# Kernel optimization log

Measured on AMD Instinct MI355X. Metric: run time of the kernel, lower is better.

## Reference

```python
import jax, jax.numpy as jnp
import numpy as np

# Ragged layout: 8 sequences packed into total_tokens=6144 tokens.
_SEQLENS = [1024, 512, 1024, 256, 768, 1024, 512, 1024]
_TOTAL = sum(_SEQLENS)  # 6144
_H, _D = 16, 128
_MAXLEN = 1024


def setup_inputs() -> dict:
    key = jax.random.key(0)
    kq, kk, kv = jax.random.split(key, 3)
    cu = jnp.asarray(np.concatenate([[0], np.cumsum(_SEQLENS)]), dtype=jnp.int32)
    return {
        "q": jax.random.normal(kq, (_TOTAL, _H, _D), dtype=jnp.float32),
        "k": jax.random.normal(kk, (_TOTAL, _H, _D), dtype=jnp.float32),
        "v": jax.random.normal(kv, (_TOTAL, _H, _D), dtype=jnp.float32),
        "cu_seqlens_q": cu,
        "cu_seqlens_k": cu,
        "max_seqlen_q": _MAXLEN,
        "max_seqlen_k": _MAXLEN,
    }


def _pad_gather(x, cu, L):
    """Gather packed [T,h,d] into padded [B,L,h,d] plus validity mask [B,L]."""
    starts = cu[:-1]                                   # [B]
    lens = cu[1:] - cu[:-1]                            # [B]
    pos = jnp.arange(L, dtype=cu.dtype)                # [L]
    idx = starts[:, None] + pos[None, :]               # [B,L]
    mask = pos[None, :] < lens[:, None]                # [B,L]
    idx = jnp.clip(idx, 0, x.shape[0] - 1)
    return x[idx], mask, jnp.where(mask, idx, x.shape[0])


def reference(q, k, v, cu_seqlens_q, cu_seqlens_k, max_seqlen_q, max_seqlen_k):
    # Equivalent to pytorch_varlen_attention: per-sequence SDPA (non-causal,
    # no dropout), vectorized via pad-to-max + key masking.
    T, h, d = q.shape
    qp, mq, idx_q = _pad_gather(q, cu_seqlens_q, max_seqlen_q)  # [B,Lq,h,d]
    kp, mk, _ = _pad_gather(k, cu_seqlens_k, max_seqlen_k)      # [B,Lk,h,d]
    vp, _, _ = _pad_gather(v, cu_seqlens_k, max_seqlen_k)

    scale = 1.0 / jnp.sqrt(jnp.asarray(d, dtype=q.dtype))
    scores = jnp.einsum("bqhd,bkhd->bhqk", qp, kp) * scale      # [B,h,Lq,Lk]
    neg = jnp.asarray(jnp.finfo(scores.dtype).min, scores.dtype)
    scores = jnp.where(mk[:, None, None, :], scores, neg)
    attn = jax.nn.softmax(scores, axis=-1)
    out_pad = jnp.einsum("bhqk,bkhd->bqhd", attn, vp)           # [B,Lq,h,d]

    # Scatter valid rows back to packed layout; invalid rows dropped (idx==T).
    out = jnp.zeros((T, h, d), dtype=q.dtype)
    out = out.at[idx_q.reshape(-1)].set(
        out_pad.reshape(-1, h, d), mode="drop")
    return out
```

## Files before the change

kernel.cpp:

```cpp
#include <hip/hip_runtime.h>
#include <hip/hip_bf16.h>
#include <stdint.h>

#define H 16
#define D 128
#define BM 256
#define BN 64
#define NW 8
#define NT 512

typedef __bf16 bf16_t;
typedef bf16_t bf16x8 __attribute__((ext_vector_type(8)));
typedef bf16_t bf16x2 __attribute__((ext_vector_type(2)));
typedef float f32x16 __attribute__((ext_vector_type(16)));

#define MFMA32(a, b, c) __builtin_amdgcn_mfma_f32_32x32x16_bf16(a, b, c, 0, 0, 0)

union FragU { uint32_t w[4]; bf16x8 v; };

static __device__ __forceinline__ uint32_t cvtpk_bf16(float lo, float hi) {
  uint32_t r;
  asm("v_cvt_pk_bf16_f32 %0, %1, %2" : "=v"(r) : "v"(lo), "v"(hi));
  return r;
}

static __device__ __forceinline__ void gld_lds16(const bf16_t* g, bf16_t* l) {
  __builtin_amdgcn_global_load_lds(
      (const __attribute__((address_space(1))) void*)g,
      (__attribute__((address_space(3))) void*)l, 16, 0, 0);
}


__global__ void conv_k(const float* __restrict__ kin, bf16_t* __restrict__ kb, int n8) {
  int i = blockIdx.x * blockDim.x + threadIdx.x;
  int stride = gridDim.x * blockDim.x;
  for (; i < n8; i += stride) {
    const float* p = kin + (size_t)i * 8;
    float4 a = *(const float4*)p, b = *(const float4*)(p + 4);
    bf16x8 w;
    w[0] = (bf16_t)a.x; w[1] = (bf16_t)a.y; w[2] = (bf16_t)a.z; w[3] = (bf16_t)a.w;
    w[4] = (bf16_t)b.x; w[5] = (bf16_t)b.y; w[6] = (bf16_t)b.z; w[7] = (bf16_t)b.w;
    *(bf16x8*)(kb + (size_t)i * 8) = w;
  }
}

__global__ void conv_vt(const float* __restrict__ v, bf16_t* __restrict__ vt,
                        const int* __restrict__ cuk, int nseq) {
  int tile = blockIdx.x, h = blockIdx.y;
  int acc = 0, seq = -1, lt = 0, s0k = 0, Lk = 0, Lkp = 0;
  size_t vb = 0;
  for (int s = 0; s < nseq; ++s) {
    int Ls = cuk[s + 1] - cuk[s];
    int Lp = (Ls + 63) & ~63;
    int nt = Lp / 64;
    if (tile < acc + nt) { seq = s; lt = tile - acc; s0k = cuk[s]; Lk = Ls; Lkp = Lp; break; }
    acc += nt; vb += (size_t)H * D * Lp;
  }
  if (seq < 0) return;
  int kv0 = lt * 64;
  int d = threadIdx.x;
  bf16x8 w[8];
  #pragma unroll
  for (int j = 0; j < 64; ++j) {
    int kv = kv0 + j;
    int kvc = kv < Lk ? kv : Lk - 1;
    float val = v[((size_t)(s0k + kvc) * H + h) * D + d];
    w[j >> 3][j & 7] = (bf16_t)val;
  }
  bf16_t* dstT = vt + vb + (size_t)h * D * Lkp + (size_t)lt * 8192;
  #pragma unroll
  for (int c = 0; c < 8; ++c)
    *(bf16x8*)(dstT + ((size_t)c * 128 + d) * 8) = w[c];
}


__global__ __launch_bounds__(NT, 2)
void fa_varlen8(const float* __restrict__ q,
                const bf16_t* __restrict__ kb,
                const bf16_t* __restrict__ vt,
                const int* __restrict__ cuq,
                const int* __restrict__ cuk,
                float* __restrict__ out,
                int nseq, int maxtiles)
{
  __shared__ alignas(16) bf16_t sK[2][BN * D];
  __shared__ alignas(16) bf16_t sVt[2][8 * 128 * 8];
  __shared__ float sRed[NW * 32];

  const int nwg = gridDim.x;
  const int orig = blockIdx.x;
  const int qq = nwg >> 3, rr = nwg & 7;
  const int xcd = orig & 7;
  const int wgid = (xcd < rr ? xcd * (qq + 1) : rr * (qq + 1) + (xcd - rr) * qq) + (orig >> 3);
  const int tile = wgid % maxtiles;
  const int h = wgid / maxtiles;

  int acc = 0, seq = -1, lt = 0, s0q = 0, s0k = 0, Lq = 0, Lk = 0, Lkp = 0;
  size_t vb = 0;
  for (int s = 0; s < nseq; ++s) {
    int a = cuq[s], b = cuq[s + 1];
    int Ls = b - a;
    int nt = (Ls + BM - 1) / BM;
    int Lks = cuk[s + 1] - cuk[s];
    int Lp = (Lks + 63) & ~63;
    if (tile < acc + nt) {
      seq = s; lt = tile - acc; s0q = a; Lq = Ls;
      s0k = cuk[s]; Lk = Lks; Lkp = Lp;
      break;
    }
    acc += nt; vb += (size_t)H * D * Lp;
  }
  if (seq < 0) return;

  const int q0 = lt * BM;
  const int tid = threadIdx.x;
  const int warp = tid >> 6;
  const int lane = tid & 63;
  const int lq = lane & 31;
  const int hi = lane >> 5;

  const float SC = 0.08838834764831845f * 1.44269504088896340f;

  bf16x8 qf[8];
  {
    int qrow = q0 + warp * 32 + lq; if (qrow >= Lq) qrow = Lq - 1;
    const float* qp = q + ((size_t)(s0q + qrow) * H + h) * D;
    #pragma unroll
    for (int ks = 0; ks < 8; ++ks) {
      const float* p = qp + ks * 16 + hi * 8;
      float4 a = *(const float4*)p, b = *(const float4*)(p + 4);
      bf16x8 r;
      r[0] = (bf16_t)(a.x * SC); r[1] = (bf16_t)(a.y * SC);
      r[2] = (bf16_t)(a.z * SC); r[3] = (bf16_t)(a.w * SC);
      r[4] = (bf16_t)(b.x * SC); r[5] = (bf16_t)(b.y * SC);
      r[6] = (bf16_t)(b.z * SC); r[7] = (bf16_t)(b.w * SC);
      qf[ks] = r;
    }
  }

  const bf16_t* vsrcH = vt + vb + (size_t)h * D * Lkp;

  auto STAGE = [&](int tt, int buf) {
    const int kvb = tt * BN;
    #pragma unroll
    for (int i = 0; i < 2; ++i) {
      int g = tid + i * NT;
      int row = g >> 4, cc = g & 15;
      int kvr = kvb + row; if (kvr >= Lk) kvr = Lk - 1;
      const bf16_t* src = kb + ((size_t)(s0k + kvr) * H + h) * D + ((cc ^ (row & 7)) << 3);
      gld_lds16(src, &sK[buf][g * 8]);
    }
    const bf16_t* vsrc = vsrcH + (size_t)tt * 8192;
    #pragma unroll
    for (int i = 0; i < 2; ++i) {
      int g = tid + i * NT;
      gld_lds16(vsrc + (size_t)g * 8, &sVt[buf][g * 8]);
    }
  };

  f32x16 oacc[4];
  #pragma unroll
  for (int dt = 0; dt < 4; ++dt)
    #pragma unroll
    for (int r = 0; r < 16; ++r) oacc[dt][r] = 0.f;
  float m = -1e30f, l = 0.f;

  const int nkv = (Lk + BN - 1) / BN;

  STAGE(0, 0);
  asm volatile("s_waitcnt vmcnt(0)" ::: "memory");
  __syncthreads();

  for (int t = 0; t < nkv; ++t) {
    const int cur = t & 1;
    const int kvb = t * BN;
    if (t + 1 < nkv) STAGE(t + 1, cur ^ 1);

    const bf16_t* sKc = sK[cur];
    const bf16_t* sVc = sVt[cur];
    const bool tail = (kvb + BN > Lk);

    #pragma unroll
    for (int ct = 0; ct < 2; ++ct) {
      f32x16 sa, sb;
      #pragma unroll
      for (int r = 0; r < 16; ++r) { sa[r] = 0.f; sb[r] = 0.f; }
      int krow = ct * 32 + lq;
      __builtin_amdgcn_s_setprio(1);
      #pragma unroll
      for (int ks = 0; ks < 4; ++ks) {
        int posa = (ks * 2 + hi) ^ (krow & 7);
        bf16x8 kfa = *(const bf16x8*)&sKc[krow * 128 + (posa << 3)];
        sa = MFMA32(kfa, qf[ks], sa);
        int posb = ((ks + 4) * 2 + hi) ^ (krow & 7);
        bf16x8 kfb = *(const bf16x8*)&sKc[krow * 128 + (posb << 3)];
        sb = MFMA32(kfb, qf[ks + 4], sb);
      }
      __builtin_amdgcn_s_setprio(0);

      f32x16 st;
      #pragma unroll
      for (int r = 0; r < 16; ++r) {
        float x = sa[r] + sb[r];
        if (tail) {
          int kvi = kvb + ct * 32 + (r & 3) + 8 * (r >> 2) + 4 * hi;
          if (kvi >= Lk) x = -1e30f;
        }
        st[r] = x;
      }
      float m0, m1;
      {
        float a0 = fmaxf(st[0], st[1]),  a1 = fmaxf(st[2], st[3]);
        float a2 = fmaxf(st[4], st[5]),  a3 = fmaxf(st[6], st[7]);
        float a4 = fmaxf(st[8], st[9]),  a5 = fmaxf(st[10], st[11]);
        float a6 = fmaxf(st[12], st[13]), a7 = fmaxf(st[14], st[15]);
        float b0 = fmaxf(a0, a1), b1 = fmaxf(a2, a3);
        float b2 = fmaxf(a4, a5), b3 = fmaxf(a6, a7);
        m0 = fmaxf(fmaxf(b0, b1), fmaxf(b2, b3));
      }
      m1 = fmaxf(m0, __shfl_xor(m0, 32));
      bool trig = m1 > m + 8.0f;
      float mnew = trig ? m1 : m;
      float alpha = __builtin_amdgcn_exp2f(m - mnew);
      m = mnew;

      #pragma unroll
      for (int r = 0; r < 16; ++r)
        st[r] = __builtin_amdgcn_exp2f(st[r] - m);
      float psum;
      {
        float a0 = st[0] + st[1],  a1 = st[2] + st[3];
        float a2 = st[4] + st[5],  a3 = st[6] + st[7];
        float a4 = st[8] + st[9],  a5 = st[10] + st[11];
        float a6 = st[12] + st[13], a7 = st[14] + st[15];
        float b0 = a0 + a1, b1 = a2 + a3, b2 = a4 + a5, b3 = a6 + a7;
        psum = (b0 + b1) + (b2 + b3);
      }
      psum += __shfl_xor(psum, 32);
      l = l * alpha + psum;

      if (__any(alpha != 1.0f)) {
        if (hi == 0) sRed[warp * 32 + lq] = alpha;
        asm volatile("s_waitcnt lgkmcnt(0)" ::: "memory");
        #pragma unroll
        for (int r = 0; r < 16; ++r) {
          float a2 = sRed[warp * 32 + (r & 3) + 8 * (r >> 2) + 4 * hi];
          #pragma unroll
          for (int dt = 0; dt < 4; ++dt) oacc[dt][r] *= a2;
        }
      }

      uint32_t c0 = cvtpk_bf16(st[0],  st[1]),  c1 = cvtpk_bf16(st[2],  st[3]);
      uint32_t c2 = cvtpk_bf16(st[4],  st[5]),  c3 = cvtpk_bf16(st[6],  st[7]);
      uint32_t c4 = cvtpk_bf16(st[8],  st[9]),  c5 = cvtpk_bf16(st[10], st[11]);
      uint32_t c6 = cvtpk_bf16(st[12], st[13]), c7 = cvtpk_bf16(st[14], st[15]);
      { auto rr2 = __builtin_amdgcn_permlane32_swap(c0, c2, false, false); c0 = rr2[0]; c2 = rr2[1]; }
      { auto rr2 = __builtin_amdgcn_permlane32_swap(c1, c3, false, false); c1 = rr2[0]; c3 = rr2[1]; }
      { auto rr2 = __builtin_amdgcn_permlane32_swap(c4, c6, false, false); c4 = rr2[0]; c6 = rr2[1]; }
      { auto rr2 = __builtin_amdgcn_permlane32_swap(c5, c7, false, false); c5 = rr2[0]; c7 = rr2[1]; }
      FragU pa, pb;
      pa.w[0] = c0; pa.w[1] = c1; pa.w[2] = c2; pa.w[3] = c3;
      pb.w[0] = c4; pb.w[1] = c5; pb.w[2] = c6; pb.w[3] = c7;

      __builtin_amdgcn_s_setprio(1);
      #pragma unroll
      for (int dt = 0; dt < 4; ++dt) {
        int drow = dt * 32 + lq;
        bf16x8 vf0 = *(const bf16x8*)&sVc[((ct * 4 + hi) * 128 + drow) << 3];
        oacc[dt] = MFMA32(pa.v, vf0, oacc[dt]);
        bf16x8 vf1 = *(const bf16x8*)&sVc[((ct * 4 + 2 + hi) * 128 + drow) << 3];
        oacc[dt] = MFMA32(pb.v, vf1, oacc[dt]);
      }
      __builtin_amdgcn_s_setprio(0);
    }

    asm volatile("s_waitcnt vmcnt(0)" ::: "memory");
    __syncthreads();
  }

  if (hi == 0) sRed[warp * 32 + lq] = l;
  asm volatile("s_waitcnt lgkmcnt(0)" ::: "memory");
  #pragma unroll
  for (int r = 0; r < 16; ++r) {
    int cr = (r & 3) + 8 * (r >> 2) + 4 * hi;
    int qr = q0 + warp * 32 + cr;
    if (qr < Lq) {
      float rn = 1.0f / sRed[warp * 32 + cr];
      float* op = out + ((size_t)(s0q + qr) * H + h) * D + lq;
      #pragma unroll
      for (int dt = 0; dt < 4; ++dt)
        op[dt * 32] = oacc[dt][r] * rn;
    }
  }
}


__global__ __launch_bounds__(256, 3)
void fa_varlen2(const float* __restrict__ q,
                const float* __restrict__ k,
                const float* __restrict__ v,
                const int* __restrict__ cuq,
                const int* __restrict__ cuk,
                float* __restrict__ out,
                int nseq)
{
  __shared__ alignas(16) bf16_t sBuf[128 * 128];
  __shared__ float sRed[4 * 32];
  bf16_t* sK  = sBuf;
  bf16_t* sVt = sBuf + 64 * 128;

  const int tile = blockIdx.x;
  const int h = blockIdx.y;

  int acc = 0, seq = -1, lt = 0, s0q = 0, s0k = 0, Lq = 0, Lk = 0;
  for (int s = 0; s < nseq; ++s) {
    int a = cuq[s], b = cuq[s + 1];
    int Ls = b - a;
    int nt = (Ls + 127) / 128;
    if (tile < acc + nt) {
      seq = s; lt = tile - acc; s0q = a; Lq = Ls;
      s0k = cuk[s]; Lk = cuk[s + 1] - s0k;
      break;
    }
    acc += nt;
  }
  if (seq < 0) return;

  const int q0 = lt * 128;
  const int tid = threadIdx.x;
  const int warp = tid >> 6;
  const int lane = tid & 63;
  const int lq = lane & 31;
  const int hi = lane >> 5;

  const float SC = 0.08838834764831845f * 1.44269504088896340f;

  #pragma unroll
  for (int ii = 0; ii < 8; ++ii) {
    int g = tid + ii * 256;
    int row = g >> 4, cc = g & 15;
    int gr = q0 + row; if (gr >= Lq) gr = Lq - 1;
    const float* p = q + ((size_t)(s0q + gr) * H + h) * D + cc * 8;
    float4 f0 = *(const float4*)p;
    float4 f1 = *(const float4*)(p + 4);
    bf16x8 w;
    w[0] = (bf16_t)f0.x; w[1] = (bf16_t)f0.y; w[2] = (bf16_t)f0.z; w[3] = (bf16_t)f0.w;
    w[4] = (bf16_t)f1.x; w[5] = (bf16_t)f1.y; w[6] = (bf16_t)f1.z; w[7] = (bf16_t)f1.w;
    *(bf16x8*)&sBuf[row * 128 + (((cc ^ (row & 7))) << 3)] = w;
  }
  __syncthreads();

  bf16x8 qf[8];
  {
    int row = warp * 32 + lq;
    #pragma unroll
    for (int ks = 0; ks < 8; ++ks) {
      int pos = (ks * 2 + hi) ^ (row & 7);
      qf[ks] = *(const bf16x8*)&sBuf[row * 128 + (pos << 3)];
    }
  }

  f32x16 oacc[4];
  #pragma unroll
  for (int dt = 0; dt < 4; ++dt)
    #pragma unroll
    for (int r = 0; r < 16; ++r) oacc[dt][r] = 0.f;
  float m = -1e30f, l = 0.f;

  const int nkv = (Lk + 63) / 64;
  for (int it = 0; it < nkv; ++it) {
    const int kv0 = it * 64;
    __syncthreads();

    #pragma unroll
    for (int ii = 0; ii < 4; ++ii) {
      int g = tid + ii * 256;
      int row = g >> 4, cc = g & 15;
      int gr = kv0 + row; if (gr >= Lk) gr = Lk - 1;
      const float* p = k + ((size_t)(s0k + gr) * H + h) * D + cc * 8;
      float4 f0 = *(const float4*)p;
      float4 f1 = *(const float4*)(p + 4);
      bf16x8 w;
      w[0] = (bf16_t)f0.x; w[1] = (bf16_t)f0.y; w[2] = (bf16_t)f0.z; w[3] = (bf16_t)f0.w;
      w[4] = (bf16_t)f1.x; w[5] = (bf16_t)f1.y; w[6] = (bf16_t)f1.z; w[7] = (bf16_t)f1.w;
      *(bf16x8*)&sK[row * 128 + (((cc ^ (row & 7))) << 3)] = w;
    }
    {
      int kp = tid & 31;
      int seg = tid >> 5;
      int r0 = kv0 + 2 * kp, r1 = r0 + 1;
      if (r0 >= Lk) r0 = Lk - 1;
      if (r1 >= Lk) r1 = Lk - 1;
      const float* p0 = v + ((size_t)(s0k + r0) * H + h) * D + seg * 16;
      const float* p1 = v + ((size_t)(s0k + r1) * H + h) * D + seg * 16;
      float va[16], vbf[16];
      *(float4*)&va[0]  = *(const float4*)p0;
      *(float4*)&va[4]  = *(const float4*)(p0 + 4);
      *(float4*)&va[8]  = *(const float4*)(p0 + 8);
      *(float4*)&va[12] = *(const float4*)(p0 + 12);
      *(float4*)&vbf[0]  = *(const float4*)p1;
      *(float4*)&vbf[4]  = *(const float4*)(p1 + 4);
      *(float4*)&vbf[8]  = *(const float4*)(p1 + 8);
      *(float4*)&vbf[12] = *(const float4*)(p1 + 12);
      int kvr = 2 * kp;
      #pragma unroll
      for (int i = 0; i < 16; ++i) {
        int d = seg * 16 + i;
        int pos = (kp >> 2) ^ (d & 7);
        bf16x2 w2; w2[0] = (bf16_t)va[i]; w2[1] = (bf16_t)vbf[i];
        *(bf16x2*)&sVt[d * 64 + (pos << 3) + (kvr & 7)] = w2;
      }
    }
    __syncthreads();

    const bool tail = (kv0 + 64 > Lk);

    #pragma unroll
    for (int ct = 0; ct < 2; ++ct) {
      f32x16 st;
      #pragma unroll
      for (int r = 0; r < 16; ++r) st[r] = 0.f;
      int krow = ct * 32 + lq;
      #pragma unroll
      for (int ks = 0; ks < 8; ++ks) {
        int pos = (ks * 2 + hi) ^ (krow & 7);
        bf16x8 kf = *(const bf16x8*)&sK[krow * 128 + (pos << 3)];
        st = MFMA32(kf, qf[ks], st);
      }

      float tmax = -1e30f;
      #pragma unroll
      for (int r = 0; r < 16; ++r) {
        float x = st[r] * SC;
        if (tail) {
          int kvi = kv0 + ct * 32 + (r & 3) + 8 * (r >> 2) + 4 * hi;
          if (kvi >= Lk) x = -1e30f;
        }
        st[r] = x;
        tmax = fmaxf(tmax, x);
      }
      tmax = fmaxf(tmax, __shfl_xor(tmax, 32));
      bool trig = tmax > m + 8.0f;
      float mnew = trig ? tmax : m;
      float alpha = exp2f(m - mnew);
      m = mnew;

      float psum = 0.f;
      #pragma unroll
      for (int r = 0; r < 16; ++r) {
        float e = exp2f(st[r] - m);
        st[r] = e;
        psum += e;
      }
      psum += __shfl_xor(psum, 32);
      l = l * alpha + psum;

      if (__any(alpha != 1.0f)) {
        if (hi == 0) sRed[warp * 32 + lq] = alpha;
        asm volatile("s_waitcnt lgkmcnt(0)" ::: "memory");
        #pragma unroll
        for (int r = 0; r < 16; ++r) {
          float a2 = sRed[warp * 32 + (r & 3) + 8 * (r >> 2) + 4 * hi];
          #pragma unroll
          for (int dt = 0; dt < 4; ++dt) oacc[dt][r] *= a2;
        }
      }

      uint32_t c0 = cvtpk_bf16(st[0],  st[1]),  c1 = cvtpk_bf16(st[2],  st[3]);
      uint32_t c2 = cvtpk_bf16(st[4],  st[5]),  c3 = cvtpk_bf16(st[6],  st[7]);
      uint32_t c4 = cvtpk_bf16(st[8],  st[9]),  c5 = cvtpk_bf16(st[10], st[11]);
      uint32_t c6 = cvtpk_bf16(st[12], st[13]), c7 = cvtpk_bf16(st[14], st[15]);
      { auto rr2 = __builtin_amdgcn_permlane32_swap(c0, c2, false, false); c0 = rr2[0]; c2 = rr2[1]; }
      { auto rr2 = __builtin_amdgcn_permlane32_swap(c1, c3, false, false); c1 = rr2[0]; c3 = rr2[1]; }
      { auto rr2 = __builtin_amdgcn_permlane32_swap(c4, c6, false, false); c4 = rr2[0]; c6 = rr2[1]; }
      { auto rr2 = __builtin_amdgcn_permlane32_swap(c5, c7, false, false); c5 = rr2[0]; c7 = rr2[1]; }
      FragU pa, pb;
      pa.w[0] = c0; pa.w[1] = c1; pa.w[2] = c2; pa.w[3] = c3;
      pb.w[0] = c4; pb.w[1] = c5; pb.w[2] = c6; pb.w[3] = c7;

      #pragma unroll
      for (int dt = 0; dt < 4; ++dt) {
        int drow = dt * 32 + lq;
        int pos0 = (ct * 4 + hi) ^ (drow & 7);
        bf16x8 vf0 = *(const bf16x8*)&sVt[drow * 64 + (pos0 << 3)];
        oacc[dt] = MFMA32(pa.v, vf0, oacc[dt]);
        int pos1 = (ct * 4 + 2 + hi) ^ (drow & 7);
        bf16x8 vf1 = *(const bf16x8*)&sVt[drow * 64 + (pos1 << 3)];
        oacc[dt] = MFMA32(pb.v, vf1, oacc[dt]);
      }
    }
  }

  if (hi == 0) sRed[warp * 32 + lq] = l;
  asm volatile("s_waitcnt lgkmcnt(0)" ::: "memory");
  #pragma unroll
  for (int r = 0; r < 16; ++r) {
    int cr = (r & 3) + 8 * (r >> 2) + 4 * hi;
    int qr = q0 + warp * 32 + cr;
    if (qr < Lq) {
      float rn = 1.0f / sRed[warp * 32 + cr];
      float* op = out + ((size_t)(s0q + qr) * H + h) * D + lq;
      #pragma unroll
      for (int dt = 0; dt < 4; ++dt)
        op[dt * 32] = oacc[dt][r] * rn;
    }
  }
}

extern "C" void kernel_launch(void* const* d_in, const int* in_sizes, int n_in,
                              void* d_out, int out_size, void* d_ws, size_t ws_size,
                              hipStream_t stream) {
  const float* q = (const float*)d_in[0];
  const float* k = (const float*)d_in[1];
  const float* v = (const float*)d_in[2];
  const int* cuq = (const int*)d_in[3];
  const int* cuk = (const int*)d_in[4];
  float* out = (float*)d_out;

  int total = in_sizes[0] / (H * D);
  int nseq = in_sizes[3] - 1;
  int maxtiles = (total + BM - 1) / BM + nseq;

  size_t needK = (size_t)in_sizes[1] * 2;
  size_t needV = (size_t)in_sizes[2] * 2 + (size_t)nseq * 64 * H * D * 2 + 256;

  if (ws_size >= needK + needV) {
    bf16_t* kb = (bf16_t*)d_ws;
    bf16_t* vtb = (bf16_t*)((char*)d_ws + needK);

    conv_k<<<1024, 256, 0, stream>>>(k, kb, in_sizes[1] / 8);
    int maxvt = (total + 63) / 64 + nseq;
    dim3 gvt(maxvt, H);
    conv_vt<<<gvt, 128, 0, stream>>>(v, vtb, cuk, nseq);
    fa_varlen8<<<dim3(maxtiles * H), NT, 0, stream>>>(q, kb, vtb, cuq, cuk, out, nseq, maxtiles);
  } else {
    int mt2 = (total + 127) / 128 + nseq;
    dim3 grid(mt2, H);
    fa_varlen2<<<grid, 256, 0, stream>>>(q, k, v, cuq, cuk, out, nseq);
  }
}
```

Before: 127.4 us.

## Give each warp two 32-row query tiles to reuse K/V LDS fragments

Halves the warps per workgroup (8 to 4) and has each warp process 64 query rows as two 32-row MFMA tiles. Each K and V fragment read from LDS now feeds two MFMAs, halving LDS read traffic per unit of compute. The cost is doubled accumulator and Q fragment registers, which may lower occupancy or cause spills, and fewer waves are available to hide latency.

```diff
diff --git a/kernel.cpp b/kernel.cpp
--- a/kernel.cpp
+++ b/kernel.cpp
@@ -6,8 +6,8 @@
 #define D 128
 #define BM 256
 #define BN 64
-#define NW 8
-#define NT 512
+#define NW 4
+#define NT 256
 
 typedef __bf16 bf16_t;
 typedef bf16_t bf16x8 __attribute__((ext_vector_type(8)));
@@ -75,7 +75,7 @@
 
 
 __global__ __launch_bounds__(NT, 2)
-void fa_varlen8(const float* __restrict__ q,
+void fa_varlen9(const float* __restrict__ q,
                 const bf16_t* __restrict__ kb,
                 const bf16_t* __restrict__ vt,
                 const int* __restrict__ cuq,
@@ -85,7 +85,7 @@
 {
   __shared__ alignas(16) bf16_t sK[2][BN * D];
   __shared__ alignas(16) bf16_t sVt[2][8 * 128 * 8];
-  __shared__ float sRed[NW * 32];
+  __shared__ float sRed[NW * 64];
 
   const int nwg = gridDim.x;
   const int orig = blockIdx.x;
@@ -121,20 +121,33 @@
 
   const float SC = 0.08838834764831845f * 1.44269504088896340f;
 
-  bf16x8 qf[8];
+  bf16x8 qf0[8], qf1[8];
   {
-    int qrow = q0 + warp * 32 + lq; if (qrow >= Lq) qrow = Lq - 1;
-    const float* qp = q + ((size_t)(s0q + qrow) * H + h) * D;
+    int qr0 = q0 + warp * 64 + lq;      if (qr0 >= Lq) qr0 = Lq - 1;
+    int qr1 = q0 + warp * 64 + 32 + lq; if (qr1 >= Lq) qr1 = Lq - 1;
+    const float* qp0 = q + ((size_t)(s0q + qr0) * H + h) * D;
+    const float* qp1 = q + ((size_t)(s0q + qr1) * H + h) * D;
     #pragma unroll
     for (int ks = 0; ks < 8; ++ks) {
-      const float* p = qp + ks * 16 + hi * 8;
-      float4 a = *(const float4*)p, b = *(const float4*)(p + 4);
+      const float* p0 = qp0 + ks * 16 + hi * 8;
+      float4 a = *(const float4*)p0, b = *(const float4*)(p0 + 4);
       bf16x8 r;
       r[0] = (bf16_t)(a.x * SC); r[1] = (bf16_t)(a.y * SC);
       r[2] = (bf16_t)(a.z * SC); r[3] = (bf16_t)(a.w * SC);
       r[4] = (bf16_t)(b.x * SC); r[5] = (bf16_t)(b.y * SC);
       r[6] = (bf16_t)(b.z * SC); r[7] = (bf16_t)(b.w * SC);
-      qf[ks] = r;
+      qf0[ks] = r;
+    }
+    #pragma unroll
+    for (int ks = 0; ks < 8; ++ks) {
+      const float* p1 = qp1 + ks * 16 + hi * 8;
+      float4 a = *(const float4*)p1, b = *(const float4*)(p1 + 4);
+      bf16x8 r;
+      r[0] = (bf16_t)(a.x * SC); r[1] = (bf16_t)(a.y * SC);
+      r[2] = (bf16_t)(a.z * SC); r[3] = (bf16_t)(a.w * SC);
+      r[4] = (bf16_t)(b.x * SC); r[5] = (bf16_t)(b.y * SC);
+      r[6] = (bf16_t)(b.z * SC); r[7] = (bf16_t)(b.w * SC);
+      qf1[ks] = r;
     }
   }
 
@@ -143,7 +156,7 @@
   auto STAGE = [&](int tt, int buf) {
     const int kvb = tt * BN;
     #pragma unroll
-    for (int i = 0; i < 2; ++i) {
+    for (int i = 0; i < 4; ++i) {
       int g = tid + i * NT;
       int row = g >> 4, cc = g & 15;
       int kvr = kvb + row; if (kvr >= Lk) kvr = Lk - 1;
@@ -152,18 +165,18 @@
     }
     const bf16_t* vsrc = vsrcH + (size_t)tt * 8192;
     #pragma unroll
-    for (int i = 0; i < 2; ++i) {
+    for (int i = 0; i < 4; ++i) {
       int g = tid + i * NT;
       gld_lds16(vsrc + (size_t)g * 8, &sVt[buf][g * 8]);
     }
   };
 
-  f32x16 oacc[4];
+  f32x16 o0[4], o1[4];
   #pragma unroll
   for (int dt = 0; dt < 4; ++dt)
     #pragma unroll
-    for (int r = 0; r < 16; ++r) oacc[dt][r] = 0.f;
-  float m = -1e30f, l = 0.f;
+    for (int r = 0; r < 16; ++r) { o0[dt][r] = 0.f; o1[dt][r] = 0.f; }
+  float m0 = -1e30f, l0 = 0.f, m1 = -1e30f, l1 = 0.f;
 
   const int nkv = (Lk + BN - 1) / BN;
 
@@ -182,94 +195,117 @@
 
     #pragma unroll
     for (int ct = 0; ct < 2; ++ct) {
-      f32x16 sa, sb;
-      #pragma unroll
-      for (int r = 0; r < 16; ++r) { sa[r] = 0.f; sb[r] = 0.f; }
+      f32x16 a0, a1;
+      #pragma unroll
+      for (int r = 0; r < 16; ++r) { a0[r] = 0.f; a1[r] = 0.f; }
       int krow = ct * 32 + lq;
       __builtin_amdgcn_s_setprio(1);
       #pragma unroll
-      for (int ks = 0; ks < 4; ++ks) {
-        int posa = (ks * 2 + hi) ^ (krow & 7);
-        bf16x8 kfa = *(const bf16x8*)&sKc[krow * 128 + (posa << 3)];
-        sa = MFMA32(kfa, qf[ks], sa);
-        int posb = ((ks + 4) * 2 + hi) ^ (krow & 7);
-        bf16x8 kfb = *(const bf16x8*)&sKc[krow * 128 + (posb << 3)];
-        sb = MFMA32(kfb, qf[ks + 4], sb);
+      for (int ks = 0; ks < 8; ++ks) {
+        int pos = (ks * 2 + hi) ^ (krow & 7);
+        bf16x8 kf = *(const bf16x8*)&sKc[krow * 128 + (pos << 3)];
+        a0 = MFMA32(kf, qf0[ks], a0);
+        a1 = MFMA32(kf, qf1[ks], a1);
       }
       __builtin_amdgcn_s_setprio(0);
 
-      f32x16 st;
+      if (tail) {
+        #pragma unroll
+        for (int r = 0; r < 16; ++r) {
+          int kvi = kvb + ct * 32 + (r & 3) + 8 * (r >> 2) + 4 * hi;
+          if (kvi >= Lk) { a0[r] = -1e30f; a1[r] = -1e30f; }
+        }
+      }
+
+      float t0, t1;
+      {
+        float x0 = fmaxf(fmaxf(fmaxf(a0[0], a0[1]), fmaxf(a0[2], a0[3])),
+                         fmaxf(fmaxf(a0[4], a0[5]), fmaxf(a0[6], a0[7])));
+        float x1 = fmaxf(fmaxf(fmaxf(a0[8], a0[9]), fmaxf(a0[10], a0[11])),
+                         fmaxf(fmaxf(a0[12], a0[13]), fmaxf(a0[14], a0[15])));
+        t0 = fmaxf(x0, x1);
+        float y0 = fmaxf(fmaxf(fmaxf(a1[0], a1[1]), fmaxf(a1[2], a1[3])),
+                         fmaxf(fmaxf(a1[4], a1[5]), fmaxf(a1[6], a1[7])));
+        float y1 = fmaxf(fmaxf(fmaxf(a1[8], a1[9]), fmaxf(a1[10], a1[11])),
+                         fmaxf(fmaxf(a1[12], a1[13]), fmaxf(a1[14], a1[15])));
+        t1 = fmaxf(y0, y1);
+      }
+      t0 = fmaxf(t0, __shfl_xor(t0, 32));
+      t1 = fmaxf(t1, __shfl_xor(t1, 32));
+      float mn0 = (t0 > m0 + 8.0f) ? t0 : m0;
+      float mn1 = (t1 > m1 + 8.0f) ? t1 : m1;
+      float alpha0 = __builtin_amdgcn_exp2f(m0 - mn0);
+      float alpha1 = __builtin_amdgcn_exp2f(m1 - mn1);
+      m0 = mn0; m1 = mn1;
+
       #pragma unroll
       for (int r = 0; r < 16; ++r) {
-        float x = sa[r] + sb[r];
-        if (tail) {
-          int kvi = kvb + ct * 32 + (r & 3) + 8 * (r >> 2) + 4 * hi;
-          if (kvi >= Lk) x = -1e30f;
-        }
-        st[r] = x;
-      }
-      float m0, m1;
+        a0[r] = __builtin_amdgcn_exp2f(a0[r] - m0);
+        a1[r] = __builtin_amdgcn_exp2f(a1[r] - m1);
+      }
+      float p0, p1;
       {
-        float a0 = fmaxf(st[0], st[1]),  a1 = fmaxf(st[2], st[3]);
-        float a2 = fmaxf(st[4], st[5]),  a3 = fmaxf(st[6], st[7]);
-        float a4 = fmaxf(st[8], st[9]),  a5 = fmaxf(st[10], st[11]);
-        float a6 = fmaxf(st[12], st[13]), a7 = fmaxf(st[14], st[15]);
-        float b0 = fmaxf(a0, a1), b1 = fmaxf(a2, a3);
-        float b2 = fmaxf(a4, a5), b3 = fmaxf(a6, a7);
-        m0 = fmaxf(fmaxf(b0, b1), fmaxf(b2, b3));
-      }
-      m1 = fmaxf(m0, __shfl_xor(m0, 32));
-      bool trig = m1 > m + 8.0f;
-      float mnew = trig ? m1 : m;
-      float alpha = __builtin_amdgcn_exp2f(m - mnew);
-      m = mnew;
-
-      #pragma unroll
-      for (int r = 0; r < 16; ++r)
-        st[r] = __builtin_amdgcn_exp2f(st[r] - m);
-      float psum;
-      {
-        float a0 = st[0] + st[1],  a1 = st[2] + st[3];
-        float a2 = st[4] + st[5],  a3 = st[6] + st[7];
-        float a4 = st[8] + st[9],  a5 = st[10] + st[11];
-        float a6 = st[12] + st[13], a7 = st[14] + st[15];
-        float b0 = a0 + a1, b1 = a2 + a3, b2 = a4 + a5, b3 = a6 + a7;
-        psum = (b0 + b1) + (b2 + b3);
-      }
-      psum += __shfl_xor(psum, 32);
-      l = l * alpha + psum;
-
-      if (__any(alpha != 1.0f)) {
-        if (hi == 0) sRed[warp * 32 + lq] = alpha;
+        float s0a = ((a0[0] + a0[1]) + (a0[2] + a0[3])) + ((a0[4] + a0[5]) + (a0[6] + a0[7]));
+        float s0b = ((a0[8] + a0[9]) + (a0[10] + a0[11])) + ((a0[12] + a0[13]) + (a0[14] + a0[15]));
+        p0 = s0a + s0b;
+        float s1a = ((a1[0] + a1[1]) + (a1[2] + a1[3])) + ((a1[4] + a1[5]) + (a1[6] + a1[7]));
+        float s1b = ((a1[8] + a1[9]) + (a1[10] + a1[11])) + ((a1[12] + a1[13]) + (a1[14] + a1[15]));
+        p1 = s1a + s1b;
+      }
+      p0 += __shfl_xor(p0, 32);
+      p1 += __shfl_xor(p1, 32);
+      l0 = l0 * alpha0 + p0;
+      l1 = l1 * alpha1 + p1;
+
+      if (__any((alpha0 != 1.0f) || (alpha1 != 1.0f))) {
+        if (hi == 0) { sRed[warp * 64 + lq] = alpha0; sRed[warp * 64 + 32 + lq] = alpha1; }
         asm volatile("s_waitcnt lgkmcnt(0)" ::: "memory");
         #pragma unroll
         for (int r = 0; r < 16; ++r) {
-          float a2 = sRed[warp * 32 + (r & 3) + 8 * (r >> 2) + 4 * hi];
+          int cr = (r & 3) + 8 * (r >> 2) + 4 * hi;
+          float b0 = sRed[warp * 64 + cr];
+          float b1 = sRed[warp * 64 + 32 + cr];
           #pragma unroll
-          for (int dt = 0; dt < 4; ++dt) oacc[dt][r] *= a2;
+          for (int dt = 0; dt < 4; ++dt) { o0[dt][r] *= b0; o1[dt][r] *= b1; }
         }
       }
 
-      uint32_t c0 = cvtpk_bf16(st[0],  st[1]),  c1 = cvtpk_bf16(st[2],  st[3]);
-      uint32_t c2 = cvtpk_bf16(st[4],  st[5]),  c3 = cvtpk_bf16(st[6],  st[7]);
-      uint32_t c4 = cvtpk_bf16(st[8],  st[9]),  c5 = cvtpk_bf16(st[10], st[11]);
-      uint32_t c6 = cvtpk_bf16(st[12], st[13]), c7 = cvtpk_bf16(st[14], st[15]);
-      { auto rr2 = __builtin_amdgcn_permlane32_swap(c0, c2, false, false); c0 = rr2[0]; c2 = rr2[1]; }
-      { auto rr2 = __builtin_amdgcn_permlane32_swap(c1, c3, false, false); c1 = rr2[0]; c3 = rr2[1]; }
-      { auto rr2 = __builtin_amdgcn_permlane32_swap(c4, c6, false, false); c4 = rr2[0]; c6 = rr2[1]; }
-      { auto rr2 = __builtin_amdgcn_permlane32_swap(c5, c7, false, false); c5 = rr2[0]; c7 = rr2[1]; }
-      FragU pa, pb;
-      pa.w[0] = c0; pa.w[1] = c1; pa.w[2] = c2; pa.w[3] = c3;
-      pb.w[0] = c4; pb.w[1] = c5; pb.w[2] = c6; pb.w[3] = c7;
+      FragU p0a, p0b, p1a, p1b;
+      {
+        uint32_t c0 = cvtpk_bf16(a0[0],  a0[1]),  c1 = cvtpk_bf16(a0[2],  a0[3]);
+        uint32_t c2 = cvtpk_bf16(a0[4],  a0[5]),  c3 = cvtpk_bf16(a0[6],  a0[7]);
+        uint32_t c4 = cvtpk_bf16(a0[8],  a0[9]),  c5 = cvtpk_bf16(a0[10], a0[11]);
+        uint32_t c6 = cvtpk_bf16(a0[12], a0[13]), c7 = cvtpk_bf16(a0[14], a0[15]);
+        { auto w2 = __builtin_amdgcn_permlane32_swap(c0, c2, false, false); c0 = w2[0]; c2 = w2[1]; }
+        { auto w2 = __builtin_amdgcn_permlane32_swap(c1, c3, false, false); c1 = w2[0]; c3 = w2[1]; }
+        { auto w2 = __builtin_amdgcn_permlane32_swap(c4, c6, false, false); c4 = w2[0]; c6 = w2[1]; }
+        { auto w2 = __builtin_amdgcn_permlane32_swap(c5, c7, false, false); c5 = w2[0]; c7 = w2[1]; }
+        p0a.w[0] = c0; p0a.w[1] = c1; p0a.w[2] = c2; p0a.w[3] = c3;
+        p0b.w[0] = c4; p0b.w[1] = c5; p0b.w[2] = c6; p0b.w[3] = c7;
+      }
+      {
+        uint32_t c0 = cvtpk_bf16(a1[0],  a1[1]),  c1 = cvtpk_bf16(a1[2],  a1[3]);
+        uint32_t c2 = cvtpk_bf16(a1[4],  a1[5]),  c3 = cvtpk_bf16(a1[6],  a1[7]);
+        uint32_t c4 = cvtpk_bf16(a1[8],  a1[9]),  c5 = cvtpk_bf16(a1[10], a1[11]);
+        uint32_t c6 = cvtpk_bf16(a1[12], a1[13]), c7 = cvtpk_bf16(a1[14], a1[15]);
+        { auto w2 = __builtin_amdgcn_permlane32_swap(c0, c2, false, false); c0 = w2[0]; c2 = w2[1]; }
+        { auto w2 = __builtin_amdgcn_permlane32_swap(c1, c3, false, false); c1 = w2[0]; c3 = w2[1]; }
+        { auto w2 = __builtin_amdgcn_permlane32_swap(c4, c6, false, false); c4 = w2[0]; c6 = w2[1]; }
+        { auto w2 = __builtin_amdgcn_permlane32_swap(c5, c7, false, false); c5 = w2[0]; c7 = w2[1]; }
+        p1a.w[0] = c0; p1a.w[1] = c1; p1a.w[2] = c2; p1a.w[3] = c3;
+        p1b.w[0] = c4; p1b.w[1] = c5; p1b.w[2] = c6; p1b.w[3] = c7;
+      }
 
       __builtin_amdgcn_s_setprio(1);
       #pragma unroll
       for (int dt = 0; dt < 4; ++dt) {
         int drow = dt * 32 + lq;
         bf16x8 vf0 = *(const bf16x8*)&sVc[((ct * 4 + hi) * 128 + drow) << 3];
-        oacc[dt] = MFMA32(pa.v, vf0, oacc[dt]);
+        o0[dt] = MFMA32(p0a.v, vf0, o0[dt]);
+        o1[dt] = MFMA32(p1a.v, vf0, o1[dt]);
         bf16x8 vf1 = *(const bf16x8*)&sVc[((ct * 4 + 2 + hi) * 128 + drow) << 3];
-        oacc[dt] = MFMA32(pb.v, vf1, oacc[dt]);
+        o0[dt] = MFMA32(p0b.v, vf1, o0[dt]);
+        o1[dt] = MFMA32(p1b.v, vf1, o1[dt]);
       }
       __builtin_amdgcn_s_setprio(0);
     }
@@ -278,18 +314,26 @@
     __syncthreads();
   }
 
-  if (hi == 0) sRed[warp * 32 + lq] = l;
+  if (hi == 0) { sRed[warp * 64 + lq] = l0; sRed[warp * 64 + 32 + lq] = l1; }
   asm volatile("s_waitcnt lgkmcnt(0)" ::: "memory");
   #pragma unroll
   for (int r = 0; r < 16; ++r) {
     int cr = (r & 3) + 8 * (r >> 2) + 4 * hi;
-    int qr = q0 + warp * 32 + cr;
-    if (qr < Lq) {
-      float rn = 1.0f / sRed[warp * 32 + cr];
-      float* op = out + ((size_t)(s0q + qr) * H + h) * D + lq;
+    int qr0 = q0 + warp * 64 + cr;
+    if (qr0 < Lq) {
+      float rn = 1.0f / sRed[warp * 64 + cr];
+      float* op = out + ((size_t)(s0q + qr0) * H + h) * D + lq;
       #pragma unroll
       for (int dt = 0; dt < 4; ++dt)
-        op[dt * 32] = oacc[dt][r] * rn;
+        op[dt * 32] = o0[dt][r] * rn;
+    }
+    int qr1 = q0 + warp * 64 + 32 + cr;
+    if (qr1 < Lq) {
+      float rn = 1.0f / sRed[warp * 64 + 32 + cr];
+      float* op = out + ((size_t)(s0q + qr1) * H + h) * D + lq;
+      #pragma unroll
+      for (int dt = 0; dt < 4; ++dt)
+        op[dt * 32] = o1[dt][r] * rn;
     }
   }
 }
@@ -532,7 +576,7 @@
     int maxvt = (total + 63) / 64 + nseq;
     dim3 gvt(maxvt, H);
     conv_vt<<<gvt, 128, 0, stream>>>(v, vtb, cuk, nseq);
-    fa_varlen8<<<dim3(maxtiles * H), NT, 0, stream>>>(q, kb, vtb, cuq, cuk, out, nseq, maxtiles);
+    fa_varlen9<<<dim3(maxtiles * H), NT, 0, stream>>>(q, kb, vtb, cuq, cuk, out, nseq, maxtiles);
   } else {
     int mt2 = (total + 127) / 128 + nseq;
     dim3 grid(mt2, H);
```

Measured after the change: 174.4 us. 37.0% more time.

## Triple-buffer K and stagger K/V prefetch with partial vmcnt waits

Applied to the files above, without the earlier changes.

Splits the tile staging into separate K and V loads, keeping K two tiles ahead in a triple buffer and V one tile ahead. The per-iteration full vmcnt(0) wait becomes vmcnt(2), so the next tile's loads stay in flight across the barrier. The LDS-based alpha and l broadcast is replaced with cross-lane shuffles, which removes the sRed buffer and its LDS waits. Cost: extra LDS for a third K buffer, which may affect occupancy, and redundant clamped loads on the final iterations.

```diff
diff --git a/kernel.cpp b/kernel.cpp
--- a/kernel.cpp
+++ b/kernel.cpp
@@ -75,17 +75,16 @@
 
 
 __global__ __launch_bounds__(NT, 2)
-void fa_varlen8(const float* __restrict__ q,
-                const bf16_t* __restrict__ kb,
-                const bf16_t* __restrict__ vt,
-                const int* __restrict__ cuq,
-                const int* __restrict__ cuk,
-                float* __restrict__ out,
-                int nseq, int maxtiles)
+void fa_varlen11(const float* __restrict__ q,
+                 const bf16_t* __restrict__ kb,
+                 const bf16_t* __restrict__ vt,
+                 const int* __restrict__ cuq,
+                 const int* __restrict__ cuk,
+                 float* __restrict__ out,
+                 int nseq, int maxtiles)
 {
-  __shared__ alignas(16) bf16_t sK[2][BN * D];
+  __shared__ alignas(16) bf16_t sK[3][BN * D];
   __shared__ alignas(16) bf16_t sVt[2][8 * 128 * 8];
-  __shared__ float sRed[NW * 32];
 
   const int nwg = gridDim.x;
   const int orig = blockIdx.x;
@@ -114,7 +113,6 @@
 
   const int q0 = lt * BM;
   const int tid = threadIdx.x;
-  const int warp = tid >> 6;
   const int lane = tid & 63;
   const int lq = lane & 31;
   const int hi = lane >> 5;
@@ -123,6 +121,7 @@
 
   bf16x8 qf[8];
   {
+    int warp = tid >> 6;
     int qrow = q0 + warp * 32 + lq; if (qrow >= Lq) qrow = Lq - 1;
     const float* qp = q + ((size_t)(s0q + qrow) * H + h) * D;
     #pragma unroll
@@ -140,7 +139,7 @@
 
   const bf16_t* vsrcH = vt + vb + (size_t)h * D * Lkp;
 
-  auto STAGE = [&](int tt, int buf) {
+  auto STAGE_K = [&](int tt, int buf) {
     const int kvb = tt * BN;
     #pragma unroll
     for (int i = 0; i < 2; ++i) {
@@ -150,6 +149,8 @@
       const bf16_t* src = kb + ((size_t)(s0k + kvr) * H + h) * D + ((cc ^ (row & 7)) << 3);
       gld_lds16(src, &sK[buf][g * 8]);
     }
+  };
+  auto STAGE_V = [&](int tt, int buf) {
     const bf16_t* vsrc = vsrcH + (size_t)tt * 8192;
     #pragma unroll
     for (int i = 0; i < 2; ++i) {
@@ -167,17 +168,22 @@
 
   const int nkv = (Lk + BN - 1) / BN;
 
-  STAGE(0, 0);
-  asm volatile("s_waitcnt vmcnt(0)" ::: "memory");
-  __syncthreads();
+  STAGE_K(0, 0);
+  STAGE_V(0, 0);
+  STAGE_K(nkv > 1 ? 1 : 0, 1);
+  asm volatile("s_waitcnt vmcnt(2)" ::: "memory");
+  __builtin_amdgcn_s_barrier();
+  __builtin_amdgcn_sched_barrier(0);
 
   for (int t = 0; t < nkv; ++t) {
-    const int cur = t & 1;
     const int kvb = t * BN;
-    if (t + 1 < nkv) STAGE(t + 1, cur ^ 1);
-
-    const bf16_t* sKc = sK[cur];
-    const bf16_t* sVc = sVt[cur];
+    int tV = t + 1 < nkv ? t + 1 : nkv - 1;
+    int tK = t + 2 < nkv ? t + 2 : nkv - 1;
+    STAGE_V(tV, (t + 1) & 1);
+    STAGE_K(tK, (t + 2) % 3);
+
+    const bf16_t* sKc = sK[t % 3];
+    const bf16_t* sVc = sVt[t & 1];
     const bool tail = (kvb + BN > Lk);
 
     #pragma unroll
@@ -208,7 +214,7 @@
         }
         st[r] = x;
       }
-      float m0, m1;
+      float m0;
       {
         float a0 = fmaxf(st[0], st[1]),  a1 = fmaxf(st[2], st[3]);
         float a2 = fmaxf(st[4], st[5]),  a3 = fmaxf(st[6], st[7]);
@@ -218,7 +224,7 @@
         float b2 = fmaxf(a4, a5), b3 = fmaxf(a6, a7);
         m0 = fmaxf(fmaxf(b0, b1), fmaxf(b2, b3));
       }
-      m1 = fmaxf(m0, __shfl_xor(m0, 32));
+      float m1 = fmaxf(m0, __shfl_xor(m0, 32));
       bool trig = m1 > m + 8.0f;
       float mnew = trig ? m1 : m;
       float alpha = __builtin_amdgcn_exp2f(m - mnew);
@@ -240,11 +246,10 @@
       l = l * alpha + psum;
 
       if (__any(alpha != 1.0f)) {
-        if (hi == 0) sRed[warp * 32 + lq] = alpha;
-        asm volatile("s_waitcnt lgkmcnt(0)" ::: "memory");
         #pragma unroll
         for (int r = 0; r < 16; ++r) {
-          float a2 = sRed[warp * 32 + (r & 3) + 8 * (r >> 2) + 4 * hi];
+          int cr = (r & 3) + 8 * (r >> 2) + 4 * hi;
+          float a2 = __shfl(alpha, cr);
           #pragma unroll
           for (int dt = 0; dt < 4; ++dt) oacc[dt][r] *= a2;
         }
@@ -274,18 +279,19 @@
       __builtin_amdgcn_s_setprio(0);
     }
 
-    asm volatile("s_waitcnt vmcnt(0)" ::: "memory");
-    __syncthreads();
-  }
-
-  if (hi == 0) sRed[warp * 32 + lq] = l;
-  asm volatile("s_waitcnt lgkmcnt(0)" ::: "memory");
+    asm volatile("s_waitcnt vmcnt(2)" ::: "memory");
+    __builtin_amdgcn_s_barrier();
+    __builtin_amdgcn_sched_barrier(0);
+  }
+
   #pragma unroll
   for (int r = 0; r < 16; ++r) {
     int cr = (r & 3) + 8 * (r >> 2) + 4 * hi;
+    int warp = tid >> 6;
     int qr = q0 + warp * 32 + cr;
+    float lcr = __shfl(l, cr);
     if (qr < Lq) {
-      float rn = 1.0f / sRed[warp * 32 + cr];
+      float rn = 1.0f / lcr;
       float* op = out + ((size_t)(s0q + qr) * H + h) * D + lq;
       #pragma unroll
       for (int dt = 0; dt < 4; ++dt)
@@ -532,7 +538,7 @@
     int maxvt = (total + 63) / 64 + nseq;
     dim3 gvt(maxvt, H);
     conv_vt<<<gvt, 128, 0, stream>>>(v, vtb, cuk, nseq);
-    fa_varlen8<<<dim3(maxtiles * H), NT, 0, stream>>>(q, kb, vtb, cuq, cuk, out, nseq, maxtiles);
+    fa_varlen11<<<dim3(maxtiles * H), NT, 0, stream>>>(q, kb, vtb, cuq, cuk, out, nseq, maxtiles);
   } else {
     int mt2 = (total + 127) / 128 + nseq;
     dim3 grid(mt2, H);
```

Result: no change. 128.8 us (+1.1%).
